# Optimization experiments

Measured on AMD Instinct MI355X. Metric: run time of the kernel, lower is better.

Reference implementation:

```python
import jax, jax.numpy as jnp
import numpy as np

THRESHOLD = 16.0
BN_EPS = 1e-5


def setup_inputs() -> dict:
    key = jax.random.key(0)
    k_x, k_w, k_b, k_g, k_be = jax.random.split(key, 5)
    B, C, H, W = 4, 128, 64, 64
    C2 = 128
    x = jax.random.normal(k_x, (B, C, H, W), dtype=jnp.float32)
    # nn.Linear(c1, c2): weight [c2, c1], bias [c2]
    W_fc = jax.random.normal(k_w, (C2, C), dtype=jnp.float32) * (1.0 / np.sqrt(C))
    b_fc = jax.random.normal(k_b, (C2,), dtype=jnp.float32) * 0.01
    # BatchNorm2d affine params
    gamma = jnp.ones((C2,), dtype=jnp.float32) + 0.1 * jax.random.normal(k_g, (C2,), dtype=jnp.float32)
    beta = 0.1 * jax.random.normal(k_be, (C2,), dtype=jnp.float32)
    return {"x": x, "W_fc": W_fc, "b_fc": b_fc, "gamma": gamma, "beta": beta}


def reference(x, W_fc, b_fc, gamma, beta):
    b, c, h, w = x.shape
    xf = x.reshape(b, c, h * w).transpose(0, 2, 1)  # [B, N, C]

    # torch.cdist(feature, feature): pairwise L2 distances [B, N, N]
    sq = jnp.sum(xf * xf, axis=-1)  # [B, N]
    d2 = sq[:, :, None] + sq[:, None, :] - 2.0 * jnp.einsum('bic,bjc->bij', xf, xf)
    dist = jnp.sqrt(jnp.maximum(d2, 0.0))
    incidence = (dist < THRESHOLD).astype(x.dtype)  # [B, N, N], N vertices x N hyperedges

    # HyPConv: fc then vertex->edge (mean) then edge->vertex (mean)
    xe = jnp.einsum('bnc,dc->bnd', xf, W_fc) + b_fc  # [B, N, c2]

    # v2e: path = incidence^T (dims 1,2); mean over incident vertices
    deg_e = jnp.sum(incidence, axis=1)  # [B, N] = row-sums of incidence^T
    edge = jnp.einsum('bve,bvc->bec', incidence, xe)  # incidence^T @ xe
    edge = jnp.where(deg_e > 0, 1.0 / deg_e, 0.0)[:, :, None] * edge

    # e2v: path = incidence; mean over incident hyperedges
    deg_v = jnp.sum(incidence, axis=2)  # [B, N]
    vert = jnp.einsum('bve,bec->bvc', incidence, edge)
    vert = jnp.where(deg_v > 0, 1.0 / deg_v, 0.0)[:, :, None] * vert

    # residual is Identity (c1 == c2)
    out = vert + xf  # [B, N, c2]
    out = out.transpose(0, 2, 1).reshape(b, -1, h, w)  # [B, c2, H, W]

    # BatchNorm2d in training mode (batch statistics, biased variance)
    mean = jnp.mean(out, axis=(0, 2, 3))
    var = jnp.var(out, axis=(0, 2, 3))
    y = (out - mean[None, :, None, None]) * jax.lax.rsqrt(var[None, :, None, None] + BN_EPS)
    y = gamma[None, :, None, None] * y + beta[None, :, None, None]
    return y * jax.nn.sigmoid(y)  # SiLU
```

## Files before the change

### kernel.cpp

```cpp
#include <hip/hip_runtime.h>
#include <hip/hip_bf16.h>

#define NB 4
#define CH 128
#define NN 4096
#define KS 4

typedef short bf16x8 __attribute__((ext_vector_type(8)));
typedef float f32x4 __attribute__((ext_vector_type(4)));
typedef float f32x16 __attribute__((ext_vector_type(16)));
using u16 = unsigned short;
using u32 = unsigned int;

__device__ __forceinline__ u16 f2bf(float v) {
  return __builtin_bit_cast(u16, __float2bfloat16(v));
}
__device__ __forceinline__ float bf2f(u16 u) {
  return __builtin_bit_cast(float, ((u32)u) << 16);
}
__device__ __forceinline__ u32 pk2(float a, float b) {
  return (u32)f2bf(a) | ((u32)f2bf(b) << 16);
}

__device__ __forceinline__ void gld16(const void* g, void* l) {
  __builtin_amdgcn_global_load_lds((const __attribute__((address_space(1))) void*)g,
                                   (__attribute__((address_space(3))) void*)l,
                                   16, 0, 0);
}

__global__ __launch_bounds__(256) void k_prep(const float* __restrict__ x,
                                              u16* __restrict__ XA,
                                              u16* __restrict__ XG) {
  __shared__ float ls[128][65];
  __shared__ float sqs[64];
  int blk = blockIdx.x;
  int b = blk >> 6;
  int n0 = (blk & 63) * 64;
  int t = threadIdx.x;
  const float* xb = x + (size_t)b * CH * NN;
  {
    int j = t & 63, cb = t >> 6;
#pragma unroll
    for (int i = 0; i < 32; ++i) {
      int c = cb * 32 + i;
      ls[c][j] = xb[(size_t)c * NN + n0 + j];
    }
  }
  __syncthreads();
  if (t < 64) {
    float s = 0.f;
#pragma unroll
    for (int c = 0; c < 128; ++c) { float v = ls[c][t]; s += v * v; }
    sqs[t] = s;
  }
  __syncthreads();
  int v = t & 31, g = t >> 5;
  const u32 one2 = 0x3F803F80u;
#pragma unroll
  for (int vt2 = 0; vt2 < 2; ++vt2) {
    int j = vt2 * 32 + v;
    float sv = sqs[j];
    u16 shi = f2bf(sv);
    u16 slo = f2bf(sv - bf2f(shi));
    size_t tb = ((size_t)b * 128 + (n0 >> 5) + vt2) * 4608;
    for (int s = g; s < 18; s += 8) {
      int k9 = s >> 1, h = s & 1;
      int c0 = k9 * 16 + h * 8;
      u32 wa[4], wg[4];
      if (k9 < 8) {
#pragma unroll
        for (int p = 0; p < 4; ++p) {
          float va = ls[c0 + 2 * p][j], vb = ls[c0 + 2 * p + 1][j];
          wa[p] = pk2(va, vb);
          wg[p] = pk2(-2.f * va, -2.f * vb);
        }
      } else if (h == 0) {
        wa[0] = (u32)shi | ((u32)slo << 16); wa[1] = one2; wa[2] = 0u; wa[3] = 0u;
        wg[0] = one2; wg[1] = (u32)shi | ((u32)slo << 16); wg[2] = 0u; wg[3] = 0u;
      } else {
        wa[0] = wa[1] = wa[2] = wa[3] = 0u;
        wg[0] = wg[1] = wg[2] = wg[3] = 0u;
      }
      *(uint4*)(XA + tb + (size_t)s * 256 + v * 8) = make_uint4(wa[0], wa[1], wa[2], wa[3]);
      *(uint4*)(XG + tb + (size_t)s * 256 + v * 8) = make_uint4(wg[0], wg[1], wg[2], wg[3]);
    }
  }
}

__global__ __launch_bounds__(256) void k_xe(const u16* __restrict__ XA,
                                            const float* __restrict__ W,
                                            const float* __restrict__ bfc,
                                            u16* __restrict__ XE2) {
  __shared__ __align__(16) char sw[32768];
  int t = threadIdx.x;
  int lane = t & 63, w = t >> 6;
  int r = lane & 31, hi = lane >> 5;
  int b = blockIdx.x >> 5, nt = blockIdx.x & 31;
  int vt = nt * 4 + w;
  {
    int d = t >> 1, half = t & 1;
    const float4* src = (const float4*)(W + (size_t)d * 128 + half * 64);
    int rowoff = d * 256, sz = (d & 7) << 4;
#pragma unroll
    for (int ch = 0; ch < 8; ++ch) {
      float4 f0 = src[ch * 2], f1 = src[ch * 2 + 1];
      *(uint4*)(sw + ((rowoff + half * 128 + ch * 16) ^ sz)) =
          make_uint4(pk2(f0.x, f0.y), pk2(f0.z, f0.w), pk2(f1.x, f1.y), pk2(f1.z, f1.w));
    }
  }
  float bias[4];
#pragma unroll
  for (int dt = 0; dt < 4; ++dt) bias[dt] = bfc[dt * 32 + r];
  __syncthreads();
  const u16* abase = XA + ((size_t)(b * 128 + vt)) * 4608;
  bf16x8 a[8];
#pragma unroll
  for (int k9 = 0; k9 < 8; ++k9)
    a[k9] = *(const bf16x8*)(abase + (k9 * 2 + hi) * 256 + r * 8);
  f32x16 acc[4];
#pragma unroll
  for (int dt = 0; dt < 4; ++dt)
#pragma unroll
    for (int q = 0; q < 16; ++q) acc[dt][q] = bias[dt];
#pragma unroll
  for (int k9 = 0; k9 < 8; ++k9) {
#pragma unroll
    for (int dt = 0; dt < 4; ++dt) {
      int d = dt * 32 + r;
      bf16x8 bf_ = *(const bf16x8*)(sw + ((d * 256 + k9 * 32 + hi * 16) ^ ((d & 7) << 4)));
      acc[dt] = __builtin_amdgcn_mfma_f32_32x32x16_bf16(a[k9], bf_, acc[dt], 0, 0, 0);
    }
  }
  u16* base = XE2 + ((size_t)(b * 128 + vt)) * 4096;
#pragma unroll
  for (int dt = 0; dt < 4; ++dt)
#pragma unroll
    for (int h = 0; h < 2; ++h)
#pragma unroll
      for (int hi2 = 0; hi2 < 2; ++hi2) {
        int q0 = h * 8 + hi2 * 4;
        u32 w0 = pk2(acc[dt][q0], acc[dt][q0 + 1]);
        u32 w1 = pk2(acc[dt][q0 + 2], acc[dt][q0 + 3]);
        *(uint2*)(base + (((dt * 2 + h) * 2 + hi2) * 32 + r) * 8 + hi * 4) =
            make_uint2(w0, w1);
      }
}

template <int MODE>
__global__ __launch_bounds__(256, 2) void k_hyp(const u16* __restrict__ XAg,
                                                const u16* __restrict__ XGg,
                                                const u16* __restrict__ B2g,
                                                u16* __restrict__ outP,
                                                float* __restrict__ deg) {
  __shared__ __align__(16) char smem[34816];
  int t = threadIdx.x;
  int lane = t & 63, w = t >> 6;
  int r = lane & 31, hi = lane >> 5;
  int bid = blockIdx.x;
  int b = bid >> 7;
  int et = (bid >> 2) & 31;
  int ks = bid & 3;
  int e0 = et * 128;
  int vt0 = ks * 32;

  bf16x8 B1[9];
  {
    const u16* g = XGg + ((size_t)(b * 128 + et * 4 + w)) * 4608 + (hi * 32 + r) * 8;
#pragma unroll
    for (int k9 = 0; k9 < 9; ++k9) B1[k9] = *(const bf16x8*)(g + k9 * 512);
  }

  f32x16 acc2[4];
#pragma unroll
  for (int dt = 0; dt < 4; ++dt)
#pragma unroll
    for (int q = 0; q < 16; ++q) acc2[dt][q] = 0.f;
  float dg = 0.f;
  f32x16 zero;
#pragma unroll
  for (int q = 0; q < 16; ++q) zero[q] = 0.f;

  const u16* xa_t = XAg + ((size_t)(b * 128 + vt0)) * 4608;
  const u16* b2_t = B2g + ((size_t)(b * 128 + vt0)) * 4096;

  {
    char* L = smem;
    for (int i = w; i < 9; i += 4) gld16(xa_t + i * 512 + lane * 8, L + i * 1024);
    for (int i = w; i < 8; i += 4) gld16(b2_t + i * 512 + lane * 8, L + 9216 + i * 1024);
  }
  int cur = 0;
  for (int tile = 0; tile < 32; ++tile) {
    if (tile + 1 < 32) {
      char* L = smem + (cur ^ 1) * 17408;
      const u16* ga = xa_t + (size_t)(tile + 1) * 4608;
      const u16* gb = b2_t + (size_t)(tile + 1) * 4096;
      for (int i = w; i < 9; i += 4) gld16(ga + i * 512 + lane * 8, L + i * 1024);
      for (int i = w; i < 8; i += 4) gld16(gb + i * 512 + lane * 8, L + 9216 + i * 1024);
      asm volatile("s_waitcnt vmcnt(4)" ::: "memory");
    } else {
      asm volatile("s_waitcnt vmcnt(0)" ::: "memory");
    }
    __builtin_amdgcn_s_barrier();
    __builtin_amdgcn_sched_barrier(0);
    char* LA = smem + cur * 17408;
    char* LB = LA + 9216;
    __builtin_amdgcn_s_setprio(1);
    f32x16 d2a, d2b;
    {
      bf16x8 a0 = *(const bf16x8*)(LA + lane * 16);
      bf16x8 a1 = *(const bf16x8*)(LA + 1024 + lane * 16);
      d2a = __builtin_amdgcn_mfma_f32_32x32x16_bf16(a0, B1[0], zero, 0, 0, 0);
      d2b = __builtin_amdgcn_mfma_f32_32x32x16_bf16(a1, B1[1], zero, 0, 0, 0);
    }
#pragma unroll
    for (int k9 = 2; k9 < 9; ++k9) {
      bf16x8 av = *(const bf16x8*)(LA + k9 * 1024 + lane * 16);
      if (k9 & 1)
        d2b = __builtin_amdgcn_mfma_f32_32x32x16_bf16(av, B1[k9], d2b, 0, 0, 0);
      else
        d2a = __builtin_amdgcn_mfma_f32_32x32x16_bf16(av, B1[k9], d2a, 0, 0, 0);
    }
    __builtin_amdgcn_s_setprio(0);
    float p[16];
#pragma unroll
    for (int q = 0; q < 16; ++q) {
      p[q] = ((d2a[q] + d2b[q]) < 256.f) ? 1.f : 0.f;
      if (MODE == 0) dg += p[q];
    }
    u32 c[8];
#pragma unroll
    for (int pr = 0; pr < 8; ++pr)
      asm("v_cvt_pk_bf16_f32 %0, %1, %2" : "=v"(c[pr]) : "v"(p[2 * pr]), "v"(p[2 * pr + 1]));
    asm volatile("v_permlane32_swap_b32 %0, %1" : "+v"(c[0]), "+v"(c[2]));
    asm volatile("v_permlane32_swap_b32 %0, %1" : "+v"(c[1]), "+v"(c[3]));
    asm volatile("v_permlane32_swap_b32 %0, %1" : "+v"(c[4]), "+v"(c[6]));
    asm volatile("v_permlane32_swap_b32 %0, %1" : "+v"(c[5]), "+v"(c[7]));
    uint4 u0 = make_uint4(c[0], c[1], c[2], c[3]);
    uint4 u1 = make_uint4(c[4], c[5], c[6], c[7]);
    bf16x8 A2h0 = __builtin_bit_cast(bf16x8, u0);
    bf16x8 A2h1 = __builtin_bit_cast(bf16x8, u1);
    __builtin_amdgcn_s_setprio(1);
#pragma unroll
    for (int dt = 0; dt < 4; ++dt) {
      bf16x8 b20 = *(const bf16x8*)(LB + dt * 2048 + hi * 512 + r * 16);
      bf16x8 b21 = *(const bf16x8*)(LB + dt * 2048 + 1024 + hi * 512 + r * 16);
      acc2[dt] = __builtin_amdgcn_mfma_f32_32x32x16_bf16(A2h0, b20, acc2[dt], 0, 0, 0);
      acc2[dt] = __builtin_amdgcn_mfma_f32_32x32x16_bf16(A2h1, b21, acc2[dt], 0, 0, 0);
    }
    __builtin_amdgcn_s_setprio(0);
    asm volatile("s_waitcnt lgkmcnt(0)" ::: "memory");
    __builtin_amdgcn_sched_barrier(0);
    __builtin_amdgcn_s_barrier();
    cur ^= 1;
  }
  if (MODE == 0) {
    float dtot = dg + __shfl_xor(dg, 32);
    if (hi == 0) atomicAdd(&deg[b * NN + e0 + w * 32 + r], dtot);
    u16* base = outP + ((size_t)(ks * NB + b) * 128 + (et * 4 + w)) * 4096;
#pragma unroll
    for (int dt = 0; dt < 4; ++dt)
#pragma unroll
      for (int h = 0; h < 2; ++h)
#pragma unroll
        for (int hi2 = 0; hi2 < 2; ++hi2) {
          int q0 = h * 8 + hi2 * 4;
          u32 w0 = pk2(acc2[dt][q0], acc2[dt][q0 + 1]);
          u32 w1 = pk2(acc2[dt][q0 + 2], acc2[dt][q0 + 3]);
          *(uint2*)(base + (((dt * 2 + h) * 2 + hi2) * 32 + r) * 8 + hi * 4) =
              make_uint2(w0, w1);
        }
  } else {
    u16* lsE = (u16*)smem + w * 4096;
#pragma unroll
    for (int dt = 0; dt < 4; ++dt)
#pragma unroll
      for (int q = 0; q < 16; ++q) {
        int e_l = (q & 3) + 8 * (q >> 2) + 4 * hi;
        lsE[e_l * 128 + dt * 32 + r] = f2bf(acc2[dt][q]);
      }
    __syncthreads();
    uint4* g4 = (uint4*)(outP + ((size_t)(ks * NB + b) * NN + e0) * 128);
    const uint4* l4 = (const uint4*)smem;
#pragma unroll
    for (int i = 0; i < 8; ++i) g4[t + i * 256] = l4[t + i * 256];
  }
}

__global__ __launch_bounds__(256) void k_escale(const u16* __restrict__ PA,
                                                const float* __restrict__ deg,
                                                u16* __restrict__ ED2) {
  int m = blockIdx.x * 256 + threadIdx.x;
#pragma unroll
  for (int it = 0; it < 2; ++it, m += 131072) {
    int g = m & 511, vt = (m >> 9) & 127, b = m >> 16;
    int hi2 = (g >> 5) & 1, h = (g >> 6) & 1;
    int e0 = vt * 32 + h * 16 + hi2 * 8;
    float4 dg0 = *(const float4*)(deg + b * NN + e0);
    float4 dg1 = *(const float4*)(deg + b * NN + e0 + 4);
    float s[8];
#pragma unroll
    for (int j = 0; j < 8; ++j) s[j] = 0.f;
    size_t off = ((size_t)(b * 128 + vt) * 512 + g) * 8;
#pragma unroll
    for (int ksv = 0; ksv < KS; ++ksv) {
      uint4 pkv = *(const uint4*)(PA + (size_t)ksv * 2097152 + off);
      u32 wv[4] = {pkv.x, pkv.y, pkv.z, pkv.w};
#pragma unroll
      for (int p = 0; p < 4; ++p) {
        s[2 * p]     += bf2f((u16)(wv[p] & 0xFFFF));
        s[2 * p + 1] += bf2f((u16)(wv[p] >> 16));
      }
    }
    float iv[8];
    iv[0] = dg0.x; iv[1] = dg0.y; iv[2] = dg0.z; iv[3] = dg0.w;
    iv[4] = dg1.x; iv[5] = dg1.y; iv[6] = dg1.z; iv[7] = dg1.w;
    u32 o[4];
#pragma unroll
    for (int p = 0; p < 4; ++p) {
      float f0 = iv[2 * p]     > 0.f ? s[2 * p]     / iv[2 * p]     : 0.f;
      float f1 = iv[2 * p + 1] > 0.f ? s[2 * p + 1] / iv[2 * p + 1] : 0.f;
      o[p] = pk2(f0, f1);
    }
    *(uint4*)(ED2 + off) = make_uint4(o[0], o[1], o[2], o[3]);
  }
}

__global__ __launch_bounds__(256) void k_vfin(const u16* __restrict__ P,
                                              const float* __restrict__ deg,
                                              const float* __restrict__ x,
                                              float* __restrict__ outp,
                                              float* __restrict__ bnsum,
                                              float* __restrict__ bnsq) {
  __shared__ float lsT[128][72];
  int blk = blockIdx.x;  int b = blk >> 6;  int n0 = (blk & 63) * 64;
  int t = threadIdx.x;
  {
    int n = t >> 2, q = t & 3;
    int i = n0 + n;
    float dv = deg[b * NN + i];
    float f = dv > 0.f ? 1.0f / dv : 0.f;
    size_t base = ((size_t)b * NN + i) * 128 + q * 32;
    float vs[32];
#pragma unroll
    for (int j = 0; j < 32; ++j) vs[j] = 0.f;
    for (int kss = 0; kss < KS; ++kss) {
      const u16* src = P + (size_t)kss * 2097152 + base;
#pragma unroll
      for (int ch = 0; ch < 4; ++ch) {
        uint4 pkv = *(const uint4*)(src + ch * 8);
        u32 wv[4] = {pkv.x, pkv.y, pkv.z, pkv.w};
#pragma unroll
        for (int pp = 0; pp < 4; ++pp) {
          vs[ch * 8 + 2 * pp]     += bf2f((u16)(wv[pp] & 0xFFFF));
          vs[ch * 8 + 2 * pp + 1] += bf2f((u16)(wv[pp] >> 16));
        }
      }
    }
#pragma unroll
    for (int j = 0; j < 32; ++j) lsT[q * 32 + j][n] = vs[j] * f;
  }
  __syncthreads();
  {
    int d = t >> 1, half = t & 1;
    const float* xr = x + ((size_t)b * CH + d) * NN + n0 + half * 32;
    float* orow = outp + ((size_t)b * CH + d) * NN + n0 + half * 32;
    float s = 0.f, s2 = 0.f;
#pragma unroll
    for (int i = 0; i < 32; ++i) {
      float v = lsT[d][half * 32 + i] + xr[i];
      orow[i] = v;
      s += v;  s2 += v * v;
    }
    s += __shfl_xor(s, 1);
    s2 += __shfl_xor(s2, 1);
    if (half == 0) { atomicAdd(&bnsum[d], s); atomicAdd(&bnsq[d], s2); }
  }
}

__global__ void k_bn(float* __restrict__ y, const float* __restrict__ bnsum,
                     const float* __restrict__ bnsq, const float* __restrict__ gamma,
                     const float* __restrict__ beta) {
  int idx = blockIdx.x * 256 + threadIdx.x;
  int d = (idx >> 12) & 127;
  const float cnt = (float)(NB * NN);
  float m = bnsum[d] / cnt;
  float var = bnsq[d] / cnt - m * m;
  float rs = rsqrtf(var + 1e-5f);
  float v = y[idx];
  float tt = (v - m) * rs * gamma[d] + beta[d];
  y[idx] = tt / (1.0f + expf(-tt));
}

extern "C" void kernel_launch(void* const* d_in, const int* in_sizes, int n_in,
                              void* d_out, int out_size, void* d_ws, size_t ws_size,
                              hipStream_t stream) {
  (void)in_sizes; (void)n_in; (void)out_size; (void)ws_size;
  const float* x     = (const float*)d_in[0];
  const float* W     = (const float*)d_in[1];
  const float* bfc   = (const float*)d_in[2];
  const float* gamma = (const float*)d_in[3];
  const float* beta  = (const float*)d_in[4];
  char* ws = (char*)d_ws;
  u16* Pbuf  = (u16*)ws;
  u16* XA    = (u16*)(ws + 33554432);
  u16* XG    = (u16*)(ws + 38273024);
  u16* XE2   = (u16*)(ws + 42991616);
  u16* ED2   = (u16*)(ws + 47185920);
  float* deg = (float*)(ws + 51380224);
  float* bnsum = (float*)(ws + 51445760);
  float* bnsq  = (float*)(ws + 51446272);

  hipMemsetAsync(ws + 51380224, 0, 66560, stream);
  k_prep<<<NB * 64, 256, 0, stream>>>(x, XA, XG);
  k_xe<<<NB * 32, 256, 0, stream>>>(XA, W, bfc, XE2);
  k_hyp<0><<<NB * 32 * KS, 256, 0, stream>>>(XA, XG, XE2, Pbuf, deg);
  k_escale<<<512, 256, 0, stream>>>(Pbuf, deg, ED2);
  k_hyp<1><<<NB * 32 * KS, 256, 0, stream>>>(XA, XG, ED2, Pbuf, deg);
  k_vfin<<<NB * 64, 256, 0, stream>>>(Pbuf, deg, x, (float*)d_out, bnsum, bnsq);
  k_bn<<<2097152 / 256, 256, 0, stream>>>((float*)d_out, bnsum, bnsq, gamma, beta);
}
```

Measured before the change: 185.6 us.

## Software-pipeline distance and aggregation MFMAs with a four-stage LDS ring

```diff
diff --git a/kernel.cpp b/kernel.cpp
--- a/kernel.cpp
+++ b/kernel.cpp
@@ -30,13 +30,15 @@
 
 __global__ __launch_bounds__(256) void k_prep(const float* __restrict__ x,
                                               u16* __restrict__ XA,
-                                              u16* __restrict__ XG) {
+                                              u16* __restrict__ XG,
+                                              float* __restrict__ zbuf) {
   __shared__ float ls[128][65];
   __shared__ float sqs[64];
   int blk = blockIdx.x;
   int b = blk >> 6;
   int n0 = (blk & 63) * 64;
   int t = threadIdx.x;
+  if (t < 65) zbuf[blk * 65 + t] = 0.f;
   const float* xb = x + (size_t)b * CH * NN;
   {
     int j = t & 63, cb = t >> 6;
@@ -146,13 +148,62 @@
       }
 }
 
+#define STAGE(tile, Lbase) do {                                              \
+    const u16* ga_ = xa_t + (size_t)(tile) * 4608;                           \
+    const u16* gb_ = b2_t + (size_t)(tile) * 4096;                           \
+    char* L_ = (Lbase);                                                      \
+    for (int i_ = w; i_ < 9; i_ += 4) gld16(ga_ + i_ * 512 + lane * 8, L_ + i_ * 1024); \
+    for (int i_ = w; i_ < 8; i_ += 4) gld16(gb_ + i_ * 512 + lane * 8, L_ + 9216 + i_ * 1024); \
+  } while (0)
+
+#define D2CHAIN(dst, Lbase) do {                                             \
+    const char* LA_ = (Lbase);                                               \
+    __builtin_amdgcn_s_setprio(1);                                           \
+    dst = __builtin_amdgcn_mfma_f32_32x32x16_bf16(                           \
+        *(const bf16x8*)(LA_ + lane * 16), B1[0], zero, 0, 0, 0);            \
+    _Pragma("unroll")                                                        \
+    for (int k9_ = 1; k9_ < 9; ++k9_)                                        \
+      dst = __builtin_amdgcn_mfma_f32_32x32x16_bf16(                         \
+          *(const bf16x8*)(LA_ + k9_ * 1024 + lane * 16), B1[k9_], dst, 0, 0, 0); \
+    __builtin_amdgcn_s_setprio(0);                                           \
+  } while (0)
+
+#define PACKPV(dd, Lbase) do {                                               \
+    const char* LB_ = (Lbase) + 9216;                                        \
+    float p_[16];                                                            \
+    _Pragma("unroll")                                                        \
+    for (int q_ = 0; q_ < 16; ++q_) {                                        \
+      p_[q_] = (dd[q_] < 256.f) ? 1.f : 0.f;                                 \
+      if (MODE == 0) dg += p_[q_];                                           \
+    }                                                                        \
+    u32 c_[8];                                                               \
+    _Pragma("unroll")                                                        \
+    for (int pr_ = 0; pr_ < 8; ++pr_)                                        \
+      asm("v_cvt_pk_bf16_f32 %0, %1, %2" : "=v"(c_[pr_]) : "v"(p_[2*pr_]), "v"(p_[2*pr_+1])); \
+    asm volatile("v_permlane32_swap_b32 %0, %1" : "+v"(c_[0]), "+v"(c_[2])); \
+    asm volatile("v_permlane32_swap_b32 %0, %1" : "+v"(c_[1]), "+v"(c_[3])); \
+    asm volatile("v_permlane32_swap_b32 %0, %1" : "+v"(c_[4]), "+v"(c_[6])); \
+    asm volatile("v_permlane32_swap_b32 %0, %1" : "+v"(c_[5]), "+v"(c_[7])); \
+    bf16x8 A2h0_ = __builtin_bit_cast(bf16x8, make_uint4(c_[0], c_[1], c_[2], c_[3])); \
+    bf16x8 A2h1_ = __builtin_bit_cast(bf16x8, make_uint4(c_[4], c_[5], c_[6], c_[7])); \
+    __builtin_amdgcn_s_setprio(1);                                           \
+    _Pragma("unroll")                                                        \
+    for (int dt_ = 0; dt_ < 4; ++dt_) {                                      \
+      bf16x8 b20_ = *(const bf16x8*)(LB_ + dt_ * 2048 + hi * 512 + r * 16);  \
+      bf16x8 b21_ = *(const bf16x8*)(LB_ + dt_ * 2048 + 1024 + hi * 512 + r * 16); \
+      acc2[dt_] = __builtin_amdgcn_mfma_f32_32x32x16_bf16(A2h0_, b20_, acc2[dt_], 0, 0, 0); \
+      acc2[dt_] = __builtin_amdgcn_mfma_f32_32x32x16_bf16(A2h1_, b21_, acc2[dt_], 0, 0, 0); \
+    }                                                                        \
+    __builtin_amdgcn_s_setprio(0);                                           \
+  } while (0)
+
 template <int MODE>
 __global__ __launch_bounds__(256, 2) void k_hyp(const u16* __restrict__ XAg,
                                                 const u16* __restrict__ XGg,
                                                 const u16* __restrict__ B2g,
                                                 u16* __restrict__ outP,
                                                 float* __restrict__ deg) {
-  __shared__ __align__(16) char smem[34816];
+  __shared__ __align__(16) char smem[69632];
   int t = threadIdx.x;
   int lane = t & 63, w = t >> 6;
   int r = lane & 31, hi = lane >> 5;
@@ -183,76 +234,40 @@
   const u16* xa_t = XAg + ((size_t)(b * 128 + vt0)) * 4608;
   const u16* b2_t = B2g + ((size_t)(b * 128 + vt0)) * 4096;
 
-  {
-    char* L = smem;
-    for (int i = w; i < 9; i += 4) gld16(xa_t + i * 512 + lane * 8, L + i * 1024);
-    for (int i = w; i < 8; i += 4) gld16(b2_t + i * 512 + lane * 8, L + 9216 + i * 1024);
-  }
-  int cur = 0;
-  for (int tile = 0; tile < 32; ++tile) {
-    if (tile + 1 < 32) {
-      char* L = smem + (cur ^ 1) * 17408;
-      const u16* ga = xa_t + (size_t)(tile + 1) * 4608;
-      const u16* gb = b2_t + (size_t)(tile + 1) * 4096;
-      for (int i = w; i < 9; i += 4) gld16(ga + i * 512 + lane * 8, L + i * 1024);
-      for (int i = w; i < 8; i += 4) gld16(gb + i * 512 + lane * 8, L + 9216 + i * 1024);
-      asm volatile("s_waitcnt vmcnt(4)" ::: "memory");
-    } else {
-      asm volatile("s_waitcnt vmcnt(0)" ::: "memory");
-    }
+  f32x16 d2X, d2Y;
+  STAGE(0, smem);
+  STAGE(1, smem + 17408);
+  STAGE(2, smem + 2 * 17408);
+  asm volatile("s_waitcnt vmcnt(3)" ::: "memory");
+  __builtin_amdgcn_s_barrier();
+  __builtin_amdgcn_sched_barrier(0);
+  D2CHAIN(d2X, smem);
+
+  for (int tt = 0; tt < 30; tt += 2) {
+    asm volatile("s_waitcnt vmcnt(3)" ::: "memory");
     __builtin_amdgcn_s_barrier();
     __builtin_amdgcn_sched_barrier(0);
-    char* LA = smem + cur * 17408;
-    char* LB = LA + 9216;
-    __builtin_amdgcn_s_setprio(1);
-    f32x16 d2a, d2b;
-    {
-      bf16x8 a0 = *(const bf16x8*)(LA + lane * 16);
-      bf16x8 a1 = *(const bf16x8*)(LA + 1024 + lane * 16);
-      d2a = __builtin_amdgcn_mfma_f32_32x32x16_bf16(a0, B1[0], zero, 0, 0, 0);
-      d2b = __builtin_amdgcn_mfma_f32_32x32x16_bf16(a1, B1[1], zero, 0, 0, 0);
-    }
-#pragma unroll
-    for (int k9 = 2; k9 < 9; ++k9) {
-      bf16x8 av = *(const bf16x8*)(LA + k9 * 1024 + lane * 16);
-      if (k9 & 1)
-        d2b = __builtin_amdgcn_mfma_f32_32x32x16_bf16(av, B1[k9], d2b, 0, 0, 0);
-      else
-        d2a = __builtin_amdgcn_mfma_f32_32x32x16_bf16(av, B1[k9], d2a, 0, 0, 0);
-    }
-    __builtin_amdgcn_s_setprio(0);
-    float p[16];
-#pragma unroll
-    for (int q = 0; q < 16; ++q) {
-      p[q] = ((d2a[q] + d2b[q]) < 256.f) ? 1.f : 0.f;
-      if (MODE == 0) dg += p[q];
-    }
-    u32 c[8];
-#pragma unroll
-    for (int pr = 0; pr < 8; ++pr)
-      asm("v_cvt_pk_bf16_f32 %0, %1, %2" : "=v"(c[pr]) : "v"(p[2 * pr]), "v"(p[2 * pr + 1]));
-    asm volatile("v_permlane32_swap_b32 %0, %1" : "+v"(c[0]), "+v"(c[2]));
-    asm volatile("v_permlane32_swap_b32 %0, %1" : "+v"(c[1]), "+v"(c[3]));
-    asm volatile("v_permlane32_swap_b32 %0, %1" : "+v"(c[4]), "+v"(c[6]));
-    asm volatile("v_permlane32_swap_b32 %0, %1" : "+v"(c[5]), "+v"(c[7]));
-    uint4 u0 = make_uint4(c[0], c[1], c[2], c[3]);
-    uint4 u1 = make_uint4(c[4], c[5], c[6], c[7]);
-    bf16x8 A2h0 = __builtin_bit_cast(bf16x8, u0);
-    bf16x8 A2h1 = __builtin_bit_cast(bf16x8, u1);
-    __builtin_amdgcn_s_setprio(1);
-#pragma unroll
-    for (int dt = 0; dt < 4; ++dt) {
-      bf16x8 b20 = *(const bf16x8*)(LB + dt * 2048 + hi * 512 + r * 16);
-      bf16x8 b21 = *(const bf16x8*)(LB + dt * 2048 + 1024 + hi * 512 + r * 16);
-      acc2[dt] = __builtin_amdgcn_mfma_f32_32x32x16_bf16(A2h0, b20, acc2[dt], 0, 0, 0);
-      acc2[dt] = __builtin_amdgcn_mfma_f32_32x32x16_bf16(A2h1, b21, acc2[dt], 0, 0, 0);
-    }
-    __builtin_amdgcn_s_setprio(0);
+    STAGE(tt + 3, smem + ((tt + 3) & 3) * 17408);
+    D2CHAIN(d2Y, smem + ((tt + 1) & 3) * 17408);
+    PACKPV(d2X, smem + (tt & 3) * 17408);
     asm volatile("s_waitcnt lgkmcnt(0)" ::: "memory");
     __builtin_amdgcn_sched_barrier(0);
+    asm volatile("s_waitcnt vmcnt(3)" ::: "memory");
     __builtin_amdgcn_s_barrier();
-    cur ^= 1;
-  }
+    __builtin_amdgcn_sched_barrier(0);
+    if (tt + 4 < 32) STAGE(tt + 4, smem + ((tt + 4) & 3) * 17408);
+    D2CHAIN(d2X, smem + ((tt + 2) & 3) * 17408);
+    PACKPV(d2Y, smem + ((tt + 1) & 3) * 17408);
+    asm volatile("s_waitcnt lgkmcnt(0)" ::: "memory");
+    __builtin_amdgcn_sched_barrier(0);
+  }
+  asm volatile("s_waitcnt vmcnt(0)" ::: "memory");
+  __builtin_amdgcn_s_barrier();
+  __builtin_amdgcn_sched_barrier(0);
+  D2CHAIN(d2Y, smem + (31 & 3) * 17408);
+  PACKPV(d2X, smem + (30 & 3) * 17408);
+  PACKPV(d2Y, smem + (31 & 3) * 17408);
+
   if (MODE == 0) {
     float dtot = dg + __shfl_xor(dg, 32);
     if (hi == 0) atomicAdd(&deg[b * NN + e0 + w * 32 + r], dtot);
@@ -270,6 +285,7 @@
               make_uint2(w0, w1);
         }
   } else {
+    __builtin_amdgcn_s_barrier();
     u16* lsE = (u16*)smem + w * 4096;
 #pragma unroll
     for (int dt = 0; dt < 4; ++dt)
@@ -410,8 +426,7 @@
   float* bnsum = (float*)(ws + 51445760);
   float* bnsq  = (float*)(ws + 51446272);
 
-  hipMemsetAsync(ws + 51380224, 0, 66560, stream);
-  k_prep<<<NB * 64, 256, 0, stream>>>(x, XA, XG);
+  k_prep<<<NB * 64, 256, 0, stream>>>(x, XA, XG, deg);
   k_xe<<<NB * 32, 256, 0, stream>>>(XA, W, bfc, XE2);
   k_hyp<0><<<NB * 32 * KS, 256, 0, stream>>>(XA, XG, XE2, Pbuf, deg);
   k_escale<<<512, 256, 0, stream>>>(Pbuf, deg, ED2);
```

Measured after the change: 175.9 us. 1.05x faster.
